# Optimization experiments

Measured on AMD Instinct MI355X. Metric: run time of the kernel, lower is better.

Reference implementation:

```python
import jax, jax.numpy as jnp
import numpy as np
from itertools import permutations

NB_OBJ = 5
DIM_BODY = 10
DIM_OBJ = 15


def _lin(k, fi, fo):
    lim = 1.0 / np.sqrt(fi)
    k1, k2 = jax.random.split(k)
    w = jax.random.uniform(k1, (fi, fo), jnp.float32, -lim, lim)
    b = jax.random.uniform(k2, (fo,), jnp.float32, -lim, lim)
    return w, b


def setup_inputs() -> dict:
    key = jax.random.key(0)
    ks = jax.random.split(key, 12)
    B = 16384
    d = {}
    d["obs"] = jax.random.normal(ks[0], (B, DIM_BODY + NB_OBJ * DIM_OBJ), jnp.float32)
    d["act"] = jax.random.normal(ks[1], (B, 4), jnp.float32)
    d["ag"] = jax.random.uniform(ks[2], (B, 30), dtype=jnp.float32)
    d["g"] = jax.random.uniform(ks[3], (B, 30), dtype=jnp.float32)
    # GnnMessagePassing: Linear(46 -> 128), relu
    d["mp_w"], d["mp_b"] = _lin(ks[4], 46, 128)
    # PhiCriticDeepSet: two parallel 2-layer MLPs (157 -> 256 -> 256), relu
    d["phi_w1"], d["phi_b1"] = _lin(ks[5], 157, 256)
    d["phi_w2"], d["phi_b2"] = _lin(ks[6], 256, 256)
    d["phi_w3"], d["phi_b3"] = _lin(ks[7], 157, 256)
    d["phi_w4"], d["phi_b4"] = _lin(ks[8], 256, 256)
    # RhoCriticDeepSet: two Linear(256 -> 1)
    d["rho_w1"], d["rho_b1"] = _lin(ks[9], 256, 1)
    d["rho_w2"], d["rho_b2"] = _lin(ks[10], 256, 1)
    edges = np.array(list(permutations(range(NB_OBJ), 2)), np.int32)  # [20, 2]
    d["edges_src"] = jnp.array(edges[:, 0])
    d["edges_dst"] = jnp.array(edges[:, 1])
    d["pred_ids"] = jnp.array([[i, (i + 10) % 30] for i in range(20)], jnp.int32)  # [20, 2]
    inc = [[j for j in range(20) if edges[j, 1] == i] for i in range(NB_OBJ)]
    d["incoming"] = jnp.array(inc, jnp.int32)  # [5, 4]
    return d


def reference(obs, act, ag, g, mp_w, mp_b, phi_w1, phi_b1, phi_w2, phi_b2,
              phi_w3, phi_b3, phi_w4, phi_b4, rho_w1, rho_b1, rho_w2, rho_b2,
              edges_src, edges_dst, pred_ids, incoming):
    B = obs.shape[0]
    E = edges_src.shape[0]
    obs_body = obs[:, :DIM_BODY]                                   # [B, 10]
    obs_obj = obs[:, DIM_BODY:].reshape(B, NB_OBJ, DIM_OBJ)        # [B, 5, 15]
    # --- message passing over the 20 directed edges ---
    delta_g = g - ag
    dg_sel = delta_g[:, pred_ids]                                  # [B, E, 2]
    src = obs_obj[:, edges_src, :]                                 # [B, E, 15]
    dst = obs_obj[:, edges_dst, :]                                 # [B, E, 15]
    base = jnp.concatenate([obs_body, act], axis=-1)               # [B, 14]
    base_e = jnp.broadcast_to(base[:, None, :], (B, E, base.shape[-1]))
    inp_mp = jnp.concatenate([base_e, dg_sel, src, dst], axis=-1)  # [B, E, 46]
    edge_feat = jax.nn.relu(jnp.einsum('bef,fo->beo', inp_mp, mp_w) + mp_b)  # [B, E, 128]
    # --- segment-sum of incoming edges per object ---
    agg = edge_feat[:, incoming, :].sum(axis=2)                    # [B, 5, 128]
    ba = jnp.concatenate([act, obs_body], axis=-1)                 # [B, 14]
    ba_n = jnp.broadcast_to(ba[:, None, :], (B, NB_OBJ, ba.shape[-1]))
    inp = jnp.concatenate([ba_n, obs_obj, agg], axis=-1)           # [B, 5, 157]
    # --- phi deep-set critics ---
    h1 = jax.nn.relu(jnp.einsum('bnf,fh->bnh', inp, phi_w1) + phi_b1)
    o1 = jax.nn.relu(h1 @ phi_w2 + phi_b2).sum(axis=1)             # [B, 256]
    h2 = jax.nn.relu(jnp.einsum('bnf,fh->bnh', inp, phi_w3) + phi_b3)
    o2 = jax.nn.relu(h2 @ phi_w4 + phi_b4).sum(axis=1)             # [B, 256]
    # --- rho heads ---
    q1 = o1 @ rho_w1 + rho_b1                                      # [B, 1]
    q2 = o2 @ rho_w2 + rho_b2                                      # [B, 1]
    return q1, q2
```

## Files before the change

kernel.cpp:

```cpp
#include <hip/hip_runtime.h>
#include <hip/hip_bf16.h>

typedef __bf16 bf16x8 __attribute__((ext_vector_type(8)));
typedef __bf16 bf16x4 __attribute__((ext_vector_type(4)));
typedef float f32x4 __attribute__((ext_vector_type(4)));

#define MFMA(a, b, c) __builtin_amdgcn_mfma_f32_16x16x32_bf16(a, b, c, 0, 0, 0)

constexpr int MP_OFF = 0;
constexpr int W1_OFF = 8192;
constexpr int W2_OFF = 49152;
constexpr int W3_OFF = 114688;
constexpr int W4_OFF = 155648;
constexpr int WS_TOTAL = 221184;
constexpr size_t WS_BYTES = (size_t)WS_TOTAL * 2;

__device__ __forceinline__ float ldf(const void* p, int i, bool f32) {
    return f32 ? ((const float*)p)[i] : (float)(((const __bf16*)p)[i]);
}
__device__ __forceinline__ int geti(const int* p, int i, bool i64) {
    return p[i64 ? 2 * i : i];
}

__global__ void detect(const unsigned short* __restrict__ uo,
                       const unsigned short* __restrict__ uw, int* __restrict__ flags) {
    int idx = blockIdx.x * 256 + threadIdx.x;
    if (idx < 8192) {
        if (((uo[idx] >> 7) & 0xFF) == 0xFF) atomicOr(&flags[0], 1);
        if (((uw[idx] >> 7) & 0xFF) == 0xFF) atomicOr(&flags[1], 1);
    }
}

__global__ void swz(const void* __restrict__ mp, const void* __restrict__ w1,
                    const void* __restrict__ w2, const void* __restrict__ w3,
                    const void* __restrict__ w4, __bf16* __restrict__ ws,
                    const int* __restrict__ flags) {
    bool f32 = flags[1] != 0;
    int idx = blockIdx.x * blockDim.x + threadIdx.x;
    if (idx >= WS_TOTAL) return;
    const void* src;
    int base, local, nKT, nsh, style, K;
    if (idx < W1_OFF)      { src = mp; base = MP_OFF; local = idx;          nKT = 2; nsh = 7; style = 0; K = 46; }
    else if (idx < W2_OFF) { src = w1; base = W1_OFF; local = idx - W1_OFF; nKT = 5; nsh = 8; style = 1; K = 157; }
    else if (idx < W3_OFF) { src = w2; base = W2_OFF; local = idx - W2_OFF; nKT = 8; nsh = 8; style = 0; K = 256; }
    else if (idx < W4_OFF) { src = w3; base = W3_OFF; local = idx - W3_OFF; nKT = 5; nsh = 8; style = 1; K = 157; }
    else                   { src = w4; base = W4_OFF; local = idx - W4_OFF; nKT = 8; nsh = 8; style = 0; K = 256; }
    int N = 1 << nsh;
    int kp = local >> nsh, n = local & (N - 1);
    int ks = kp;
    bool ok = true;
    if (style == 1) { if (kp >= 32) ks = kp - 3; else if (kp >= 29) ok = false; }
    if (ks >= K) ok = false;
    float v = ok ? ldf(src, ks * N + n, f32) : 0.f;
    int dst = ((n >> 4) * nKT + (kp >> 5)) * 512 +
              (((((kp >> 3) & 3)) << 4) | (n & 15)) * 8 + (kp & 7);
    ws[base + dst] = (__bf16)v;
}

__device__ __forceinline__ bf16x8 gatherB(const void* W, bool f32, int style,
                                          int K, int N, int k0, int n, int q) {
    bf16x8 r;
#pragma unroll
    for (int j = 0; j < 8; ++j) {
        int k = k0 + q * 8 + j;
        bool ok = true;
        if (style == 1) { if (k >= 32) k -= 3; else if (k >= 29) ok = false; }
        if (k >= K) ok = false;
        float v = ok ? ldf(W, k * N + n, f32) : 0.f;
        r[j] = (__bf16)v;
    }
    return r;
}

template <int PC, int PBASE>
__device__ __forceinline__ void buildA(__bf16* sA, const __bf16* rb, const int* s_esrc,
                                       const int* s_pid0, const int* s_pid1, int tid) {
    for (int i = tid; i < 16 * PC * 8; i += 512) {
        int r = i >> 3, oct = i & 7;
        int lb = r / PC, p = PBASE + r % PC;
        const __bf16* row = rb + lb * 120;
        bf16x8 v;
#pragma unroll
        for (int j = 0; j < 8; ++j) {
            int k = oct * 8 + j;
            __bf16 x = (__bf16)0.f;
            if (k < 10) x = row[k];
            else if (k < 14) x = row[85 + (k - 10)];
            else if (k < 16) x = row[89 + ((k == 14) ? s_pid0[p] : s_pid1[p])];
            else if (k < 31) x = row[10 + s_esrc[p] * 15 + (k - 16)];
            else if (k < 46) x = row[10 + (p >> 2) * 15 + (k - 31)];
            v[j] = x;
        }
        int t = (r >> 4) * 2 + (oct >> 2);
        int lanep = ((oct & 3) << 4) | (r & 15);
        *(bf16x8*)(sA + t * 512 + lanep * 8) = v;
    }
}

template <int PC, int PBASE, bool DW>
__device__ __forceinline__ void stage1(const __bf16* Wf, const void* Wn, bool fW,
                                       const void* mp_b, const __bf16* sA,
                                       __bf16* s_inp, int wave, int lane) {
    int q = lane >> 4, c = lane & 15;
    int nt = wave;
    float mb = ldf(mp_b, nt * 16 + c, fW);
    f32x4 zero4 = {0.f, 0.f, 0.f, 0.f};
#pragma unroll
    for (int mtg = 0; mtg < PC / 4; ++mtg) {
        f32x4 acc[4];
#pragma unroll
        for (int m = 0; m < 4; ++m) acc[m] = zero4;
#pragma unroll
        for (int kt = 0; kt < 2; ++kt) {
            bf16x8 bw;
            if constexpr (DW) bw = gatherB(Wn, fW, 0, 46, 128, kt * 32, nt * 16 + c, q);
            else bw = *(const bf16x8*)(Wf + (nt * 2 + kt) * 512 + lane * 8);
#pragma unroll
            for (int m = 0; m < 4; ++m) {
                bf16x8 a = *(const bf16x8*)(sA + ((mtg * 4 + m) * 2 + kt) * 512 + lane * 8);
                acc[m] = MFMA(a, bw, acc[m]);
            }
        }
#pragma unroll
        for (int m = 0; m < 4; ++m) {
            int mt = mtg * 4 + m;
            float sum = 0.f;
#pragma unroll
            for (int rr = 0; rr < 4; ++rr) {
                float z = acc[m][rr] + mb;
                sum += (z > 0.f) ? z : 0.f;
            }
            int r0 = mt * 16 + q * 4;
            int lb = r0 / PC;
            int o = (PBASE + (r0 % PC)) >> 2;
            int rinp = lb * 5 + o;
            int kk = 32 + nt * 16 + c;
            s_inp[((rinp >> 4) * 5 + (kk >> 5)) * 512 +
                  ((((kk & 31) >> 3) << 4) + (rinp & 15)) * 8 + (kk & 7)] = (__bf16)sum;
        }
    }
}

template <int MTN, bool DW>
__device__ __forceinline__ void stage2s(int mbase, const __bf16* Wf, const void* Wn,
                                        bool fW, const void* Ba, __bf16* s_h,
                                        const __bf16* s_inp, int wave, int lane) {
    int q = lane >> 4, c = lane & 15;
    f32x4 zero4 = {0.f, 0.f, 0.f, 0.f};
    float bias_r[2][4];
#pragma unroll
    for (int n = 0; n < 2; ++n)
#pragma unroll
        for (int rg = 0; rg < 4; ++rg)
            bias_r[n][rg] = ldf(Ba, (wave * 2 + n) * 16 + q * 4 + rg, fW);
#pragma unroll
    for (int n = 0; n < 2; ++n) {
        int ht = wave * 2 + n;
        bf16x8 aw[5];
#pragma unroll
        for (int kt = 0; kt < 5; ++kt) {
            if constexpr (DW) aw[kt] = gatherB(Wn, fW, 1, 157, 256, kt * 32, ht * 16 + c, q);
            else aw[kt] = *(const bf16x8*)(Wf + (ht * 5 + kt) * 512 + lane * 8);
        }
        f32x4 acc[MTN];
#pragma unroll
        for (int m = 0; m < MTN; ++m) acc[m] = zero4;
#pragma unroll
        for (int kt = 0; kt < 5; ++kt) {
#pragma unroll
            for (int m = 0; m < MTN; ++m) {
                bf16x8 b = *(const bf16x8*)(s_inp + ((mbase + m) * 5 + kt) * 512 + lane * 8);
                acc[m] = MFMA(aw[kt], b, acc[m]);
            }
        }
#pragma unroll
        for (int m = 0; m < MTN; ++m) {
            bf16x4 hv;
#pragma unroll
            for (int rg = 0; rg < 4; ++rg) {
                float z = acc[m][rg] + bias_r[n][rg];
                hv[rg] = (__bf16)((z > 0.f) ? z : 0.f);
            }
            *(bf16x4*)(s_h + (m * 8 + (ht >> 1)) * 512 +
                       ((((ht & 1) * 2 + (q >> 1)) << 4) | c) * 8 + ((q & 1) << 2)) = hv;
        }
    }
}

template <int MTN, bool DW>
__device__ __forceinline__ void stage3s(int mbase, const __bf16* Wf, const void* Wn,
                                        bool fW, const void* Bb, const void* Rh,
                                        const __bf16* s_h, float* s_qp, int wave, int lane) {
    int q = lane >> 4, c = lane & 15;
    f32x4 zero4 = {0.f, 0.f, 0.f, 0.f};
    float bias_r[2][4], rho_r[2][4];
#pragma unroll
    for (int n = 0; n < 2; ++n)
#pragma unroll
        for (int rg = 0; rg < 4; ++rg) {
            int ncol = (wave * 2 + n) * 16 + q * 4 + rg;
            bias_r[n][rg] = ldf(Bb, ncol, fW);
            rho_r[n][rg] = ldf(Rh, ncol, fW);
        }
    float rowsum[MTN];
#pragma unroll
    for (int m = 0; m < MTN; ++m) rowsum[m] = 0.f;
#pragma unroll
    for (int n = 0; n < 2; ++n) {
        int nt = wave * 2 + n;
        bf16x8 aw[8];
#pragma unroll
        for (int kt = 0; kt < 8; ++kt) {
            if constexpr (DW) aw[kt] = gatherB(Wn, fW, 0, 256, 256, kt * 32, nt * 16 + c, q);
            else aw[kt] = *(const bf16x8*)(Wf + (nt * 8 + kt) * 512 + lane * 8);
        }
        f32x4 acc[MTN];
#pragma unroll
        for (int m = 0; m < MTN; ++m) acc[m] = zero4;
#pragma unroll
        for (int kt = 0; kt < 8; ++kt) {
#pragma unroll
            for (int m = 0; m < MTN; ++m) {
                bf16x8 b = *(const bf16x8*)(s_h + (m * 8 + kt) * 512 + lane * 8);
                acc[m] = MFMA(aw[kt], b, acc[m]);
            }
        }
#pragma unroll
        for (int m = 0; m < MTN; ++m)
#pragma unroll
            for (int rg = 0; rg < 4; ++rg) {
                float z = acc[m][rg] + bias_r[n][rg];
                z = (z > 0.f) ? z : 0.f;
                rowsum[m] += z * rho_r[n][rg];
            }
    }
#pragma unroll
    for (int m = 0; m < MTN; ++m) {
        float v = rowsum[m];
        v += __shfl_xor(v, 16);
        v += __shfl_xor(v, 32);
        if (q == 0) {
            int r0 = (mbase + m) * 16 + c;
            atomicAdd(&s_qp[r0 / 5], v);
        }
    }
}

template <bool DW>
__global__ __launch_bounds__(512, 4) void gn_main(
    const void* __restrict__ obs, const void* __restrict__ act,
    const void* __restrict__ ag, const void* __restrict__ g,
    const void* __restrict__ mp_b, const void* __restrict__ b1,
    const void* __restrict__ b2, const void* __restrict__ b3,
    const void* __restrict__ b4, const void* __restrict__ rw1,
    const void* __restrict__ rb1, const void* __restrict__ rw2,
    const void* __restrict__ rb2, const int* __restrict__ eA,
    const int* __restrict__ eB, const int* __restrict__ pred_ids,
    const int* __restrict__ incoming, const __bf16* __restrict__ wsW,
    const void* __restrict__ mp_w, const void* __restrict__ w1,
    const void* __restrict__ w2, const void* __restrict__ w3,
    const void* __restrict__ w4, const int* __restrict__ flags,
    float* __restrict__ out, int Btot) {
    __shared__ __align__(16) __bf16 s_union[14208];
    __shared__ __align__(16) __bf16 s_inp[12800];
    __shared__ int s_esrc[20], s_pid0[20], s_pid1[20];

    int tid = threadIdx.x, lane = tid & 63, wave = tid >> 6;
    __bf16* rb = s_union + 12288;
    float* s_q = (float*)(s_union + 12288);
    int b0 = blockIdx.x * 16;

    bool fI, fW;
    if constexpr (DW) {
        const unsigned short* uo = (const unsigned short*)obs;
        const unsigned short* uw = (const unsigned short*)w2;
        int d0 = 0, d1 = 0;
        for (int i = lane; i < 8192; i += 64) {
            if (((uo[i] >> 7) & 0xFF) == 0xFF) d0 = 1;
            if (((uw[i] >> 7) & 0xFF) == 0xFF) d1 = 1;
        }
        fI = __ballot(d0) != 0;
        fW = __ballot(d1) != 0;
    } else {
        fI = flags[0] != 0;
        fW = flags[1] != 0;
    }

    bool i64_i = (incoming[1] == 0);
    bool i64_p = (pred_ids[1] == 0);
    bool i64_e = (eA[9] == 0);
    const int* es = (geti(eA, 4, i64_e) == 1) ? eA : eB;

    if (tid < 20) {
        int e = geti(incoming, tid, i64_i);
        s_esrc[tid] = geti(es, e, i64_e);
        s_pid0[tid] = geti(pred_ids, 2 * e, i64_p);
        s_pid1[tid] = geti(pred_ids, 2 * e + 1, i64_p);
    }

    for (int i = tid; i < 16 * 120; i += 512) {
        int lb = i / 120, cidx = i % 120;
        int bg = b0 + lb;
        float v = 0.f;
        if (cidx < 85) v = ldf(obs, bg * 85 + cidx, fI);
        else if (cidx < 89) v = ldf(act, bg * 4 + (cidx - 85), fI);
        else if (cidx < 119) {
            int t = cidx - 89;
            v = ldf(g, bg * 30 + t, fI) - ldf(ag, bg * 30 + t, fI);
        }
        rb[i] = (__bf16)v;
    }
    __syncthreads();

    for (int i = tid; i < 80 * 4; i += 512) {
        int r = i >> 2, oct = i & 3;
        int lb = r / 5, o = r % 5;
        const __bf16* row = rb + lb * 120;
        bf16x8 v;
#pragma unroll
        for (int j = 0; j < 8; ++j) {
            int k = oct * 8 + j;
            __bf16 x = (__bf16)0.f;
            if (k < 4) x = row[85 + k];
            else if (k < 14) x = row[k - 4];
            else if (k < 29) x = row[10 + o * 15 + (k - 14)];
            v[j] = x;
        }
        *(bf16x8*)(s_inp + (r >> 4) * 2560 + ((oct << 4) | (r & 15)) * 8) = v;
    }
    buildA<12, 0>(s_union, rb, s_esrc, s_pid0, s_pid1, tid);
    __syncthreads();
    stage1<12, 0, DW>(wsW + MP_OFF, mp_w, fW, mp_b, s_union, s_inp, wave, lane);
    __syncthreads();
    buildA<8, 12>(s_union, rb, s_esrc, s_pid0, s_pid1, tid);
    __syncthreads();
    if (tid < 32) s_q[tid] = 0.f;
    stage1<8, 12, DW>(wsW + MP_OFF, mp_w, fW, mp_b, s_union, s_inp, wave, lane);
    __syncthreads();

    for (int P = 0; P < 2; ++P) {
        const __bf16* Wa = wsW + (P ? W3_OFF : W1_OFF);
        const __bf16* Wb = wsW + (P ? W4_OFF : W2_OFF);
        const void* Wan = P ? w3 : w1;
        const void* Wbn = P ? w4 : w2;
        const void* ba = P ? b3 : b1;
        const void* bb = P ? b4 : b2;
        const void* rho = P ? rw2 : rw1;
        float* qp = s_q + P * 16;
        stage2s<3, DW>(0, Wa, Wan, fW, ba, s_union, s_inp, wave, lane);
        __syncthreads();
        stage3s<3, DW>(0, Wb, Wbn, fW, bb, rho, s_union, qp, wave, lane);
        __syncthreads();
        stage2s<2, DW>(3, Wa, Wan, fW, ba, s_union, s_inp, wave, lane);
        __syncthreads();
        stage3s<2, DW>(3, Wb, Wbn, fW, bb, rho, s_union, qp, wave, lane);
        __syncthreads();
    }

    if (tid < 16) {
        out[b0 + tid] = s_q[tid] + ldf(rb1, 0, fW);
        out[Btot + b0 + tid] = s_q[16 + tid] + ldf(rb2, 0, fW);
    }
}

extern "C" void kernel_launch(void* const* d_in, const int* in_sizes, int n_in,
                              void* d_out, int out_size, void* d_ws, size_t ws_size,
                              hipStream_t stream) {
    int B = out_size / 2;

    const void *obs = nullptr, *act = nullptr, *ag = nullptr, *g = nullptr;
    const void *mp_w = nullptr, *mp_b = nullptr;
    const void *w1 = nullptr, *b1 = nullptr, *w2 = nullptr, *b2 = nullptr;
    const void *w3 = nullptr, *b3 = nullptr, *w4 = nullptr, *b4 = nullptr;
    const void *rw1 = nullptr, *rb1 = nullptr, *rw2 = nullptr, *rb2 = nullptr;
    const int *eA = nullptr, *eB = nullptr, *pred = nullptr, *inc = nullptr;
    int c30 = 0, c256 = 0, c1 = 0, c40k = 0, c65k = 0, c20 = 0;
    for (int i = 0; i < n_in; ++i) {
        int sz = in_sizes[i];
        const void* p = d_in[i];
        if (sz == B * 85) obs = p;
        else if (sz == B * 30) { if (c30++ == 0) ag = p; else g = p; }
        else if (sz == 5888) mp_w = p;
        else if (sz == 128) mp_b = p;
        else if (sz == 40192) { if (c40k++ == 0) w1 = p; else w3 = p; }
        else if (sz == 65536 || sz == B * 4) {
            int c = c65k++;
            if (c == 0) act = p; else if (c == 1) w2 = p; else w4 = p;
        }
        else if (sz == 256) {
            int c = c256++;
            if (c == 0) b1 = p; else if (c == 1) b2 = p; else if (c == 2) b3 = p;
            else if (c == 3) b4 = p; else if (c == 4) rw1 = p; else rw2 = p;
        }
        else if (sz == 1) { if (c1++ == 0) rb1 = p; else rb2 = p; }
        else if (sz == 40) pred = (const int*)p;
        else if (sz == 20) {
            int c = c20++;
            if (c == 0) eA = (const int*)p;
            else if (c == 1) eB = (const int*)p;
            else inc = (const int*)p;
        }
    }
    if (!obs || !act || !ag || !g || !mp_w || !mp_b || !w1 || !b1 || !w2 || !b2 ||
        !w3 || !b3 || !w4 || !b4 || !rw1 || !rb1 || !rw2 || !rb2 || !eA || !eB ||
        !pred || !inc) {
        obs = d_in[0]; act = d_in[1]; ag = d_in[2]; g = d_in[3];
        mp_w = d_in[4]; mp_b = d_in[5]; w1 = d_in[6]; b1 = d_in[7];
        w2 = d_in[8]; b2 = d_in[9]; w3 = d_in[10]; b3 = d_in[11];
        w4 = d_in[12]; b4 = d_in[13]; rw1 = d_in[14]; rb1 = d_in[15];
        rw2 = d_in[16]; rb2 = d_in[17];
        eA = (const int*)d_in[18]; eB = (const int*)d_in[19];
        pred = (const int*)d_in[20]; inc = (const int*)d_in[21];
    }

    float* out = (float*)d_out;
    __bf16* wsW = (__bf16*)d_ws;
    bool use_ws = ws_size >= WS_BYTES + 8;
    int* flags = (int*)((char*)d_ws + WS_BYTES);
    int grid = B / 16;

    if (use_ws) {
        hipMemsetAsync(flags, 0, 8, stream);
        detect<<<32, 256, 0, stream>>>((const unsigned short*)obs,
                                       (const unsigned short*)w2, flags);
        swz<<<(WS_TOTAL + 255) / 256, 256, 0, stream>>>(mp_w, w1, w2, w3, w4, wsW, flags);
        gn_main<false><<<grid, 512, 0, stream>>>(
            obs, act, ag, g, mp_b, b1, b2, b3, b4, rw1, rb1, rw2, rb2,
            eA, eB, pred, inc, wsW, mp_w, w1, w2, w3, w4, flags, out, B);
    } else {
        gn_main<true><<<grid, 512, 0, stream>>>(
            obs, act, ag, g, mp_b, b1, b2, b3, b4, rw1, rb1, rw2, rb2,
            eA, eB, pred, inc, wsW, mp_w, w1, w2, w3, w4, flags, out, B);
    }
}
```

Before: 178.1 us.

## Fold dtype detection into swizzle, shrink LDS, hoist weight fragments, raise occupancy

Folds the dtype-detection kernel and the memset into the swizzle kernel: every block rescans the w2 sample itself and block 0 also scans obs and writes the flags, which removes two launches. The stage-2 and stage-3 GEMMs now loop over K on the outside, load each weight fragment once per k-tile and keep two N-tiles of accumulators live. Stage 1 hoists the message-weight fragments out of the M loop, and the edge pass is split into three chunks (8/8/4) so the A buffer fits in a smaller shared array. Launch bounds go from 4 to 6 blocks per CU, and the A-build loops are remapped so consecutive threads write consecutive 16-byte lanes. The risk is register pressure from the larger accumulator arrays under the tighter occupancy bound, plus redundant global reads for detection in every swizzle block.

```diff
diff --git a/kernel.cpp b/kernel.cpp
--- a/kernel.cpp
+++ b/kernel.cpp
@@ -22,21 +22,30 @@
     return p[i64 ? 2 * i : i];
 }
 
-__global__ void detect(const unsigned short* __restrict__ uo,
-                       const unsigned short* __restrict__ uw, int* __restrict__ flags) {
-    int idx = blockIdx.x * 256 + threadIdx.x;
-    if (idx < 8192) {
-        if (((uo[idx] >> 7) & 0xFF) == 0xFF) atomicOr(&flags[0], 1);
-        if (((uw[idx] >> 7) & 0xFF) == 0xFF) atomicOr(&flags[1], 1);
-    }
-}
-
 __global__ void swz(const void* __restrict__ mp, const void* __restrict__ w1,
                     const void* __restrict__ w2, const void* __restrict__ w3,
                     const void* __restrict__ w4, __bf16* __restrict__ ws,
-                    const int* __restrict__ flags) {
-    bool f32 = flags[1] != 0;
-    int idx = blockIdx.x * blockDim.x + threadIdx.x;
+                    const unsigned short* __restrict__ uo, int* __restrict__ flags) {
+    __shared__ int s_fw, s_fi;
+    int tid = threadIdx.x;
+    if (tid == 0) { s_fw = 0; s_fi = 0; }
+    __syncthreads();
+    const unsigned short* uw = (const unsigned short*)w2;
+    int d = 0;
+    for (int i = tid; i < 8192; i += 256)
+        d |= (((uw[i] >> 7) & 0xFF) == 0xFF) ? 1 : 0;
+    if (d) atomicOr(&s_fw, 1);
+    if (blockIdx.x == 0) {
+        int d0 = 0;
+        for (int i = tid; i < 8192; i += 256)
+            d0 |= (((uo[i] >> 7) & 0xFF) == 0xFF) ? 1 : 0;
+        if (d0) atomicOr(&s_fi, 1);
+    }
+    __syncthreads();
+    bool f32 = s_fw != 0;
+    if (blockIdx.x == 0 && tid == 0) { flags[0] = s_fi; flags[1] = s_fw; }
+
+    int idx = blockIdx.x * blockDim.x + tid;
     if (idx >= WS_TOTAL) return;
     const void* src;
     int base, local, nKT, nsh, style, K;
@@ -76,7 +85,9 @@
 __device__ __forceinline__ void buildA(__bf16* sA, const __bf16* rb, const int* s_esrc,
                                        const int* s_pid0, const int* s_pid1, int tid) {
     for (int i = tid; i < 16 * PC * 8; i += 512) {
-        int r = i >> 3, oct = i & 7;
+        int t = i >> 6, lanep = i & 63;
+        int oct = ((t & 1) << 2) | (lanep >> 4);
+        int r = (t >> 1) * 16 + (lanep & 15);
         int lb = r / PC, p = PBASE + r % PC;
         const __bf16* row = rb + lb * 120;
         bf16x8 v;
@@ -91,8 +102,6 @@
             else if (k < 46) x = row[10 + (p >> 2) * 15 + (k - 31)];
             v[j] = x;
         }
-        int t = (r >> 4) * 2 + (oct >> 2);
-        int lanep = ((oct & 3) << 4) | (r & 15);
         *(bf16x8*)(sA + t * 512 + lanep * 8) = v;
     }
 }
@@ -104,40 +113,34 @@
     int q = lane >> 4, c = lane & 15;
     int nt = wave;
     float mb = ldf(mp_b, nt * 16 + c, fW);
+    bf16x8 bw[2];
+#pragma unroll
+    for (int kt = 0; kt < 2; ++kt) {
+        if constexpr (DW) bw[kt] = gatherB(Wn, fW, 0, 46, 128, kt * 32, nt * 16 + c, q);
+        else bw[kt] = *(const bf16x8*)(Wf + (nt * 2 + kt) * 512 + lane * 8);
+    }
     f32x4 zero4 = {0.f, 0.f, 0.f, 0.f};
 #pragma unroll
-    for (int mtg = 0; mtg < PC / 4; ++mtg) {
-        f32x4 acc[4];
-#pragma unroll
-        for (int m = 0; m < 4; ++m) acc[m] = zero4;
+    for (int m = 0; m < PC; ++m) {
+        f32x4 acc = zero4;
 #pragma unroll
         for (int kt = 0; kt < 2; ++kt) {
-            bf16x8 bw;
-            if constexpr (DW) bw = gatherB(Wn, fW, 0, 46, 128, kt * 32, nt * 16 + c, q);
-            else bw = *(const bf16x8*)(Wf + (nt * 2 + kt) * 512 + lane * 8);
-#pragma unroll
-            for (int m = 0; m < 4; ++m) {
-                bf16x8 a = *(const bf16x8*)(sA + ((mtg * 4 + m) * 2 + kt) * 512 + lane * 8);
-                acc[m] = MFMA(a, bw, acc[m]);
-            }
-        }
-#pragma unroll
-        for (int m = 0; m < 4; ++m) {
-            int mt = mtg * 4 + m;
-            float sum = 0.f;
-#pragma unroll
-            for (int rr = 0; rr < 4; ++rr) {
-                float z = acc[m][rr] + mb;
-                sum += (z > 0.f) ? z : 0.f;
-            }
-            int r0 = mt * 16 + q * 4;
-            int lb = r0 / PC;
-            int o = (PBASE + (r0 % PC)) >> 2;
-            int rinp = lb * 5 + o;
-            int kk = 32 + nt * 16 + c;
-            s_inp[((rinp >> 4) * 5 + (kk >> 5)) * 512 +
-                  ((((kk & 31) >> 3) << 4) + (rinp & 15)) * 8 + (kk & 7)] = (__bf16)sum;
-        }
+            bf16x8 a = *(const bf16x8*)(sA + (m * 2 + kt) * 512 + lane * 8);
+            acc = MFMA(a, bw[kt], acc);
+        }
+        float sum = 0.f;
+#pragma unroll
+        for (int rr = 0; rr < 4; ++rr) {
+            float z = acc[rr] + mb;
+            sum += (z > 0.f) ? z : 0.f;
+        }
+        int r0 = m * 16 + q * 4;
+        int lb = r0 / PC;
+        int o = (PBASE + r0 % PC) >> 2;
+        int rinp = lb * 5 + o;
+        int kk = 32 + nt * 16 + c;
+        s_inp[((rinp >> 4) * 5 + (kk >> 5)) * 512 +
+              ((((kk & 31) >> 3) << 4) + (rinp & 15)) * 8 + (kk & 7)] = (__bf16)sum;
     }
 }
 
@@ -147,6 +150,27 @@
                                         const __bf16* s_inp, int wave, int lane) {
     int q = lane >> 4, c = lane & 15;
     f32x4 zero4 = {0.f, 0.f, 0.f, 0.f};
+    f32x4 acc[2][MTN];
+#pragma unroll
+    for (int n = 0; n < 2; ++n)
+#pragma unroll
+        for (int m = 0; m < MTN; ++m) acc[n][m] = zero4;
+#pragma unroll
+    for (int kt = 0; kt < 5; ++kt) {
+        bf16x8 b[MTN];
+#pragma unroll
+        for (int m = 0; m < MTN; ++m)
+            b[m] = *(const bf16x8*)(s_inp + ((mbase + m) * 5 + kt) * 512 + lane * 8);
+#pragma unroll
+        for (int n = 0; n < 2; ++n) {
+            int ht = wave * 2 + n;
+            bf16x8 aw;
+            if constexpr (DW) aw = gatherB(Wn, fW, 1, 157, 256, kt * 32, ht * 16 + c, q);
+            else aw = *(const bf16x8*)(Wf + (ht * 5 + kt) * 512 + lane * 8);
+#pragma unroll
+            for (int m = 0; m < MTN; ++m) acc[n][m] = MFMA(aw, b[m], acc[n][m]);
+        }
+    }
     float bias_r[2][4];
 #pragma unroll
     for (int n = 0; n < 2; ++n)
@@ -156,29 +180,12 @@
 #pragma unroll
     for (int n = 0; n < 2; ++n) {
         int ht = wave * 2 + n;
-        bf16x8 aw[5];
-#pragma unroll
-        for (int kt = 0; kt < 5; ++kt) {
-            if constexpr (DW) aw[kt] = gatherB(Wn, fW, 1, 157, 256, kt * 32, ht * 16 + c, q);
-            else aw[kt] = *(const bf16x8*)(Wf + (ht * 5 + kt) * 512 + lane * 8);
-        }
-        f32x4 acc[MTN];
-#pragma unroll
-        for (int m = 0; m < MTN; ++m) acc[m] = zero4;
-#pragma unroll
-        for (int kt = 0; kt < 5; ++kt) {
-#pragma unroll
-            for (int m = 0; m < MTN; ++m) {
-                bf16x8 b = *(const bf16x8*)(s_inp + ((mbase + m) * 5 + kt) * 512 + lane * 8);
-                acc[m] = MFMA(aw[kt], b, acc[m]);
-            }
-        }
 #pragma unroll
         for (int m = 0; m < MTN; ++m) {
             bf16x4 hv;
 #pragma unroll
             for (int rg = 0; rg < 4; ++rg) {
-                float z = acc[m][rg] + bias_r[n][rg];
+                float z = acc[n][m][rg] + bias_r[n][rg];
                 hv[rg] = (__bf16)((z > 0.f) ? z : 0.f);
             }
             *(bf16x4*)(s_h + (m * 8 + (ht >> 1)) * 512 +
@@ -193,6 +200,27 @@
                                         const __bf16* s_h, float* s_qp, int wave, int lane) {
     int q = lane >> 4, c = lane & 15;
     f32x4 zero4 = {0.f, 0.f, 0.f, 0.f};
+    f32x4 acc[2][MTN];
+#pragma unroll
+    for (int n = 0; n < 2; ++n)
+#pragma unroll
+        for (int m = 0; m < MTN; ++m) acc[n][m] = zero4;
+#pragma unroll
+    for (int kt = 0; kt < 8; ++kt) {
+        bf16x8 b[MTN];
+#pragma unroll
+        for (int m = 0; m < MTN; ++m)
+            b[m] = *(const bf16x8*)(s_h + (m * 8 + kt) * 512 + lane * 8);
+#pragma unroll
+        for (int n = 0; n < 2; ++n) {
+            int nt = wave * 2 + n;
+            bf16x8 aw;
+            if constexpr (DW) aw = gatherB(Wn, fW, 0, 256, 256, kt * 32, nt * 16 + c, q);
+            else aw = *(const bf16x8*)(Wf + (nt * 8 + kt) * 512 + lane * 8);
+#pragma unroll
+            for (int m = 0; m < MTN; ++m) acc[n][m] = MFMA(aw, b[m], acc[n][m]);
+        }
+    }
     float bias_r[2][4], rho_r[2][4];
 #pragma unroll
     for (int n = 0; n < 2; ++n)
@@ -206,34 +234,15 @@
 #pragma unroll
     for (int m = 0; m < MTN; ++m) rowsum[m] = 0.f;
 #pragma unroll
-    for (int n = 0; n < 2; ++n) {
-        int nt = wave * 2 + n;
-        bf16x8 aw[8];
-#pragma unroll
-        for (int kt = 0; kt < 8; ++kt) {
-            if constexpr (DW) aw[kt] = gatherB(Wn, fW, 0, 256, 256, kt * 32, nt * 16 + c, q);
-            else aw[kt] = *(const bf16x8*)(Wf + (nt * 8 + kt) * 512 + lane * 8);
-        }
-        f32x4 acc[MTN];
-#pragma unroll
-        for (int m = 0; m < MTN; ++m) acc[m] = zero4;
-#pragma unroll
-        for (int kt = 0; kt < 8; ++kt) {
-#pragma unroll
-            for (int m = 0; m < MTN; ++m) {
-                bf16x8 b = *(const bf16x8*)(s_h + (m * 8 + kt) * 512 + lane * 8);
-                acc[m] = MFMA(aw[kt], b, acc[m]);
-            }
-        }
+    for (int n = 0; n < 2; ++n)
 #pragma unroll
         for (int m = 0; m < MTN; ++m)
 #pragma unroll
             for (int rg = 0; rg < 4; ++rg) {
-                float z = acc[m][rg] + bias_r[n][rg];
+                float z = acc[n][m][rg] + bias_r[n][rg];
                 z = (z > 0.f) ? z : 0.f;
                 rowsum[m] += z * rho_r[n][rg];
             }
-    }
 #pragma unroll
     for (int m = 0; m < MTN; ++m) {
         float v = rowsum[m];
@@ -247,7 +256,7 @@
 }
 
 template <bool DW>
-__global__ __launch_bounds__(512, 4) void gn_main(
+__global__ __launch_bounds__(512, 6) void gn_main(
     const void* __restrict__ obs, const void* __restrict__ act,
     const void* __restrict__ ag, const void* __restrict__ g,
     const void* __restrict__ mp_b, const void* __restrict__ b1,
@@ -261,13 +270,13 @@
     const void* __restrict__ w2, const void* __restrict__ w3,
     const void* __restrict__ w4, const int* __restrict__ flags,
     float* __restrict__ out, int Btot) {
-    __shared__ __align__(16) __bf16 s_union[14208];
+    __shared__ __align__(16) __bf16 s_union[12288];
     __shared__ __align__(16) __bf16 s_inp[12800];
+    __shared__ __align__(16) float s_q[32];
     __shared__ int s_esrc[20], s_pid0[20], s_pid1[20];
 
     int tid = threadIdx.x, lane = tid & 63, wave = tid >> 6;
-    __bf16* rb = s_union + 12288;
-    float* s_q = (float*)(s_union + 12288);
+    __bf16* rb = s_union + 8192;
     int b0 = blockIdx.x * 16;
 
     bool fI, fW;
@@ -312,8 +321,10 @@
     }
     __syncthreads();
 
-    for (int i = tid; i < 80 * 4; i += 512) {
-        int r = i >> 2, oct = i & 3;
+    for (int i = tid; i < 320; i += 512) {
+        int mt = i >> 6, lanep = i & 63;
+        int oct = lanep >> 4;
+        int r = mt * 16 + (lanep & 15);
         int lb = r / 5, o = r % 5;
         const __bf16* row = rb + lb * 120;
         bf16x8 v;
@@ -326,16 +337,20 @@
             else if (k < 29) x = row[10 + o * 15 + (k - 14)];
             v[j] = x;
         }
-        *(bf16x8*)(s_inp + (r >> 4) * 2560 + ((oct << 4) | (r & 15)) * 8) = v;
-    }
-    buildA<12, 0>(s_union, rb, s_esrc, s_pid0, s_pid1, tid);
-    __syncthreads();
-    stage1<12, 0, DW>(wsW + MP_OFF, mp_w, fW, mp_b, s_union, s_inp, wave, lane);
-    __syncthreads();
-    buildA<8, 12>(s_union, rb, s_esrc, s_pid0, s_pid1, tid);
-    __syncthreads();
+        *(bf16x8*)(s_inp + mt * 2560 + lanep * 8) = v;
+    }
+    buildA<8, 0>(s_union, rb, s_esrc, s_pid0, s_pid1, tid);
+    __syncthreads();
+    stage1<8, 0, DW>(wsW + MP_OFF, mp_w, fW, mp_b, s_union, s_inp, wave, lane);
+    __syncthreads();
+    buildA<8, 8>(s_union, rb, s_esrc, s_pid0, s_pid1, tid);
+    __syncthreads();
+    stage1<8, 8, DW>(wsW + MP_OFF, mp_w, fW, mp_b, s_union, s_inp, wave, lane);
+    __syncthreads();
+    buildA<4, 16>(s_union, rb, s_esrc, s_pid0, s_pid1, tid);
+    __syncthreads();
+    stage1<4, 16, DW>(wsW + MP_OFF, mp_w, fW, mp_b, s_union, s_inp, wave, lane);
     if (tid < 32) s_q[tid] = 0.f;
-    stage1<8, 12, DW>(wsW + MP_OFF, mp_w, fW, mp_b, s_union, s_inp, wave, lane);
     __syncthreads();
 
     for (int P = 0; P < 2; ++P) {
@@ -420,10 +435,8 @@
     int grid = B / 16;
 
     if (use_ws) {
-        hipMemsetAsync(flags, 0, 8, stream);
-        detect<<<32, 256, 0, stream>>>((const unsigned short*)obs,
-                                       (const unsigned short*)w2, flags);
-        swz<<<(WS_TOTAL + 255) / 256, 256, 0, stream>>>(mp_w, w1, w2, w3, w4, wsW, flags);
+        swz<<<(WS_TOTAL + 255) / 256, 256, 0, stream>>>(
+            mp_w, w1, w2, w3, w4, wsW, (const unsigned short*)obs, flags);
         gn_main<false><<<grid, 512, 0, stream>>>(
             obs, act, ag, g, mp_b, b1, b2, b3, b4, rw1, rb1, rw2, rb2,
             eA, eB, pred, inc, wsW, mp_w, w1, w2, w3, w4, flags, out, B);
```

Result: no change. 178.7 us, median of 2 (+0.4%).
